# Kernel optimization log

Hardware: AMD Instinct MI355X
Metric: run time of the kernel (lower is better)

The kernel has to match this reference:

```python
import jax, jax.numpy as jnp
import numpy as np

EPS = 1e-9
ROUTINGS = 3
B, H, CIN, COUT = 16, 8, 32, 32


def setup_inputs() -> dict:
    key = jax.random.key(0)
    k1, k2 = jax.random.split(key)
    # activations/poses from a previous capsule layer are in [0,1) after squashing/sigmoid
    x = jax.random.uniform(k1, (B, H, H, CIN * 17), dtype=jnp.float32)
    w = jax.random.normal(k2, (1, CIN, COUT, 4, 4), dtype=jnp.float32)  # TruncatedNormal(std=1) ~ normal
    beta_v = jnp.zeros((COUT, 18), jnp.float32)
    beta_a = jnp.zeros((COUT,), jnp.float32)
    ij = jnp.stack(jnp.meshgrid(jnp.arange(H), jnp.arange(H), indexing='ij'), axis=-1)
    coord_add = ij.reshape(H * H, 2).astype(jnp.float32) / H  # [H*H, 2] scaled coords
    return {"x": x, "w": w, "beta_v": beta_v, "beta_a": beta_a, "coord_add": coord_add}


def em_routing(votes, activation, beta_v, beta_a, routings):
    # votes: [N, ci, co, ch=18], activation: [N, ci, 1]
    N, ci, co, ch = votes.shape
    r = jnp.full((N, ci, co), 1.0 / co, dtype=votes.dtype)
    miu = sigma_sq = act_out = None
    for it in range(routings):  # small fixed routing count
        if it > 0:
            # E-step: Gaussian log-likelihood of each vote under each output capsule
            log_p = -0.5 * jnp.log(sigma_sq) - jnp.square(votes - miu) / (2.0 * sigma_sq)  # [N,ci,co,ch]
            log_p = log_p - (jnp.max(log_p, axis=(2, 3), keepdims=True) - jnp.log(10.0))
            p = jnp.exp(jnp.sum(log_p, axis=3))  # [N,ci,co]
            ap = p * act_out.reshape(N, 1, co)
            r = ap / (jnp.sum(ap, axis=2, keepdims=True) + EPS)
        # M-step
        r = r * activation  # weight by input activation, broadcast over co
        r = r / (jnp.sum(r, axis=2, keepdims=True) + EPS)
        r_sum = jnp.sum(r, axis=1, keepdims=True)  # [N,1,co]
        r1 = (r / (r_sum + EPS))[..., None]        # [N,ci,co,1]
        miu = jnp.sum(votes * r1, axis=1, keepdims=True)                        # [N,1,co,ch]
        sigma_sq = jnp.sum(jnp.square(votes - miu) * r1, axis=1, keepdims=True) + EPS
        if it == routings - 1:
            rs = r_sum.reshape(N, co, 1)
            cost_h = (beta_v + 0.5 * jnp.log(sigma_sq.reshape(N, co, ch))) * rs  # [N,co,ch]
            ac_lambda = 0.01 * (it + 1)
            act_out = jax.nn.softmax(ac_lambda * (beta_a - jnp.sum(cost_h, axis=2)), axis=-1)
        else:
            act_out = jax.nn.softmax(r_sum.reshape(N, co), axis=-1)
    return miu, act_out


def reference(x, w, beta_v, beta_a, coord_add):
    Bx, Hx, Wx, C = x.shape
    ci = C // 17
    xr = x.reshape(Bx, Hx, Wx, ci, 17)
    pose = xr[..., :16].reshape(-1, ci, 16)   # [N, ci, 16], N = B*H*W
    act = xr[..., 16].reshape(-1, ci, 1)      # [N, ci, 1]
    N = pose.shape[0]
    co = w.shape[2]
    # mat_transform: batched 4x4 matmul pose @ w per (input capsule, output capsule)
    votes = jnp.einsum('niab,icbd->nicad', pose.reshape(N, ci, 4, 4), w[0]).reshape(N, ci, co, 16)
    # coordinate addition: 2 extra channels with spatial coords, tiled over batch/capsules
    coord = jnp.broadcast_to(coord_add.reshape(Hx * Wx, 1, 1, 2), (Hx * Wx, ci, co, 2))
    coord = jnp.tile(coord, (Bx, 1, 1, 1))    # [N, ci, co, 2]
    votes = jnp.concatenate([coord, votes], axis=3)  # [N, ci, co, 18]
    miu, act_out = em_routing(votes, act, beta_v, beta_a, ROUTINGS)
    # global average pool over the spatial grid
    outputs = jnp.mean(act_out.reshape(Bx, Hx, Wx, co), axis=(1, 2))                       # [B, co]
    pose_out = jnp.mean(miu.reshape(Bx, Hx, Wx, co * 18), axis=(1, 2)).reshape(Bx, co, 18)  # [B, co, 18]
    return outputs, pose_out
```

## Files before the change

### kernel.cpp

```cpp
#include <hip/hip_runtime.h>
#include <math.h>


#define CI 32
#define CO 32
#define CH 18
#define NPOS 1024
#define SP 19
#define OUT_ACT (16 * CO)

constexpr float EPSF = 1e-9f;
constexpr float LN10 = 2.302585092994046f;

__global__ __launch_bounds__(256) void zero_out_kernel(float* __restrict__ out, int n) {
    int i = blockIdx.x * 256 + threadIdx.x;
    if (i < n) out[i] = 0.0f;
}

__device__ __forceinline__ float bf_max32(float x) {
    #pragma unroll
    for (int m = 16; m >= 1; m >>= 1) x = fmaxf(x, __shfl_xor(x, m));
    return x;
}
__device__ __forceinline__ float bf_sum32(float x) {
    #pragma unroll
    for (int m = 16; m >= 1; m >>= 1) x += __shfl_xor(x, m);
    return x;
}

__global__ __launch_bounds__(256) void caps_em_kernel(
    const float* __restrict__ x,
    const float* __restrict__ w,
    const float* __restrict__ beta_v,
    const float* __restrict__ beta_a,
    const float* __restrict__ coord_add,
    float* __restrict__ out)
{
    const int n  = blockIdx.x;
    const int t  = threadIdx.x;
    const int c  = t & 31;
    const int ig = t >> 5;

    __shared__ float pose[CI][16];
    __shared__ float act_in[CI];
    __shared__ float P[8][CO];
    __shared__ float partial[8][CO * SP];
    __shared__ float miu_s[CO * SP];
    __shared__ float lsig_s[CO * SP];
    __shared__ float inv2_s[CO * SP];

    const float* xrow = x + n * (CI * 17);
    for (int e = t; e < CI * 17; e += 256) {
        int i = e / 17, k = e % 17;
        float val = xrow[e];
        if (k < 16) pose[i][k] = val;
        else        act_in[i]  = val;
    }
    const float cx = coord_add[(n & 63) * 2 + 0];
    const float cy = coord_add[(n & 63) * 2 + 1];
    __syncthreads();

    float v[4][16];
    float a_in[4];
    #pragma unroll
    for (int k = 0; k < 4; ++k) {
        int i = ig * 4 + k;
        a_in[k] = act_in[i];
        float pr[16], wr[16];
        const float4* pp4 = (const float4*)pose[i];
        const float4* wp4 = (const float4*)(w + ((i * CO + c) << 4));
        #pragma unroll
        for (int q = 0; q < 4; ++q) {
            float4 pf = pp4[q];
            pr[q*4+0] = pf.x; pr[q*4+1] = pf.y; pr[q*4+2] = pf.z; pr[q*4+3] = pf.w;
            float4 wf = wp4[q];
            wr[q*4+0] = wf.x; wr[q*4+1] = wf.y; wr[q*4+2] = wf.z; wr[q*4+3] = wf.w;
        }
        #pragma unroll
        for (int a = 0; a < 4; ++a) {
            #pragma unroll
            for (int d = 0; d < 4; ++d) {
                float s = pr[a*4+0] * wr[0*4+d];
                s += pr[a*4+1] * wr[1*4+d];
                s += pr[a*4+2] * wr[2*4+d];
                s += pr[a*4+3] * wr[3*4+d];
                v[k][a*4+d] = s;
            }
        }
    }

    float rr[4];
    float act_c = 0.0f;

    for (int it = 0; it < 3; ++it) {
        if (it > 0) {
            #pragma unroll
            for (int k = 0; k < 4; ++k) {
                float S = 0.0f, mx = -3.0e38f;
                #pragma unroll
                for (int ch = 0; ch < CH; ++ch) {
                    float vv = (ch == 0) ? cx : ((ch == 1) ? cy : v[k][ch - 2]);
                    float d  = vv - miu_s[c * SP + ch];
                    float lp = -0.5f * lsig_s[c * SP + ch] - d * d * inv2_s[c * SP + ch];
                    S += lp;
                    mx = fmaxf(mx, lp);
                }
                float m = bf_max32(mx);
                float shift = 18.0f * (m - LN10);
                float p  = expf(S - shift);
                float ap = p * act_c;
                float A  = bf_sum32(ap);
                float re = ap / (A + EPSF);
                float sk = A / (A + EPSF);
                float an = a_in[k];
                rr[k] = re * an / (an * sk + EPSF);
            }
        } else {
            #pragma unroll
            for (int k = 0; k < 4; ++k) {
                float an = a_in[k];
                rr[k] = (1.0f / 32.0f) * an / (an + EPSF);
            }
        }

        P[ig][c] = rr[0] + rr[1] + rr[2] + rr[3];
        __syncthreads();
        float r_sum = 0.0f;
        #pragma unroll
        for (int g = 0; g < 8; ++g) r_sum += P[g][c];
        float denom = r_sum + EPSF;
        float r1[4], r1s = 0.0f;
        #pragma unroll
        for (int k = 0; k < 4; ++k) { r1[k] = rr[k] / denom; r1s += r1[k]; }

        {
            float* pp = &partial[ig][c * SP];
            pp[0] = cx * r1s;
            pp[1] = cy * r1s;
            #pragma unroll
            for (int ch = 2; ch < CH; ++ch)
                pp[ch] = v[0][ch-2]*r1[0] + v[1][ch-2]*r1[1]
                       + v[2][ch-2]*r1[2] + v[3][ch-2]*r1[3];
        }
        __syncthreads();
        for (int e = t; e < CO * SP; e += 256) {
            float s = 0.0f;
            #pragma unroll
            for (int g = 0; g < 8; ++g) s += partial[g][e];
            miu_s[e] = s;
        }
        __syncthreads();

        {
            float* pp = &partial[ig][c * SP];
            float d0 = cx - miu_s[c * SP + 0];
            float d1 = cy - miu_s[c * SP + 1];
            pp[0] = d0 * d0 * r1s;
            pp[1] = d1 * d1 * r1s;
            #pragma unroll
            for (int ch = 2; ch < CH; ++ch) {
                float mu = miu_s[c * SP + ch];
                float e0 = v[0][ch-2]-mu, e1 = v[1][ch-2]-mu;
                float e2 = v[2][ch-2]-mu, e3 = v[3][ch-2]-mu;
                pp[ch] = e0*e0*r1[0] + e1*e1*r1[1] + e2*e2*r1[2] + e3*e3*r1[3];
            }
        }
        __syncthreads();
        for (int e = t; e < CO * SP; e += 256) {
            float s = 0.0f;
            #pragma unroll
            for (int g = 0; g < 8; ++g) s += partial[g][e];
            s += EPSF;
            lsig_s[e] = logf(s);
            inv2_s[e] = 0.5f / s;
        }
        __syncthreads();

        float logit;
        if (it == 2) {
            float cost = 0.0f;
            #pragma unroll
            for (int ch = 0; ch < CH; ++ch)
                cost += beta_v[c * CH + ch] + 0.5f * lsig_s[c * SP + ch];
            logit = 0.03f * (beta_a[c] - cost * r_sum);
        } else {
            logit = r_sum;
        }
        float mx = bf_max32(logit);
        float ex = expf(logit - mx);
        float sden = bf_sum32(ex);
        act_c = ex / sden;
    }

    const float inv64 = 1.0f / 64.0f;
    const int b = n >> 6;
    if (t < CO) atomicAdd(&out[b * CO + t], act_c * inv64);
    for (int e = t; e < CO * CH; e += 256) {
        int cc = e / CH, ch = e - cc * CH;
        atomicAdd(&out[OUT_ACT + b * (CO * CH) + e], miu_s[cc * SP + ch] * inv64);
    }
}

extern "C" void kernel_launch(void* const* d_in, const int* in_sizes, int n_in,
                              void* d_out, int out_size, void* d_ws, size_t ws_size,
                              hipStream_t stream) {
    const float* x         = (const float*)d_in[0];
    const float* w         = (const float*)d_in[1];
    const float* beta_v    = (const float*)d_in[2];
    const float* beta_a    = (const float*)d_in[3];
    const float* coord_add = (const float*)d_in[4];
    float* out = (float*)d_out;

    zero_out_kernel<<<dim3((out_size + 255) / 256), dim3(256), 0, stream>>>(out, out_size);
    caps_em_kernel<<<dim3(NPOS), dim3(256), 0, stream>>>(
        x, w, beta_v, beta_a, coord_add, out);
}
```

Measured before the change: 93.27 us.

## Fuse mean and variance into one pass via raw moments, cut barriers

The M-step now accumulates unnormalised first and second moments in a single pass. Variance is computed as E[v^2]-mu^2 with a correction factor, which removes one reduce round and two barriers per iteration. Partial sums are pre-combined across half-waves with shuffles, so shared memory holds 4 slices instead of 8. The E-step loop is reordered to load each channel's shared values once for all four capsules, fast __expf/__logf intrinsics are used, and the zeroing kernel is replaced by hipMemsetAsync. The one-pass variance can lose precision through cancellation, which the clamp to zero only partly masks.

```diff
diff --git a/kernel.cpp b/kernel.cpp
--- a/kernel.cpp
+++ b/kernel.cpp
@@ -6,16 +6,12 @@
 #define CO 32
 #define CH 18
 #define NPOS 1024
-#define SP 19
+#define PSTR 38
+#define MSTR 19
 #define OUT_ACT (16 * CO)
 
 constexpr float EPSF = 1e-9f;
 constexpr float LN10 = 2.302585092994046f;
-
-__global__ __launch_bounds__(256) void zero_out_kernel(float* __restrict__ out, int n) {
-    int i = blockIdx.x * 256 + threadIdx.x;
-    if (i < n) out[i] = 0.0f;
-}
 
 __device__ __forceinline__ float bf_max32(float x) {
     #pragma unroll
@@ -40,14 +36,14 @@
     const int t  = threadIdx.x;
     const int c  = t & 31;
     const int ig = t >> 5;
+    const int wv = t >> 6;
 
     __shared__ float pose[CI][16];
     __shared__ float act_in[CI];
-    __shared__ float P[8][CO];
-    __shared__ float partial[8][CO * SP];
-    __shared__ float miu_s[CO * SP];
-    __shared__ float lsig_s[CO * SP];
-    __shared__ float inv2_s[CO * SP];
+    __shared__ float part[4][CO * PSTR];
+    __shared__ float miu_s[CO * MSTR];
+    __shared__ float lsig_s[CO * MSTR];
+    __shared__ float inv2_s[CO * MSTR];
 
     const float* xrow = x + n * (CI * 17);
     for (int e = t; e < CI * 17; e += 256) {
@@ -94,24 +90,32 @@
 
     for (int it = 0; it < 3; ++it) {
         if (it > 0) {
+            float S[4]  = {0.0f, 0.0f, 0.0f, 0.0f};
+            float mx[4] = {-3.0e38f, -3.0e38f, -3.0e38f, -3.0e38f};
+            #pragma unroll
+            for (int ch = 0; ch < CH; ++ch) {
+                float mu   = miu_s[c * MSTR + ch];
+                float base = -0.5f * lsig_s[c * MSTR + ch];
+                float q    = inv2_s[c * MSTR + ch];
+                #pragma unroll
+                for (int k = 0; k < 4; ++k) {
+                    float vv = (ch == 0) ? cx : ((ch == 1) ? cy : v[k][ch - 2]);
+                    float d  = vv - mu;
+                    float lp = base - d * d * q;
+                    S[k] += lp;
+                    mx[k] = fmaxf(mx[k], lp);
+                }
+            }
             #pragma unroll
             for (int k = 0; k < 4; ++k) {
-                float S = 0.0f, mx = -3.0e38f;
-                #pragma unroll
-                for (int ch = 0; ch < CH; ++ch) {
-                    float vv = (ch == 0) ? cx : ((ch == 1) ? cy : v[k][ch - 2]);
-                    float d  = vv - miu_s[c * SP + ch];
-                    float lp = -0.5f * lsig_s[c * SP + ch] - d * d * inv2_s[c * SP + ch];
-                    S += lp;
-                    mx = fmaxf(mx, lp);
-                }
-                float m = bf_max32(mx);
+                float m = bf_max32(mx[k]);
                 float shift = 18.0f * (m - LN10);
-                float p  = expf(S - shift);
+                float p  = __expf(S[k] - shift);
                 float ap = p * act_c;
                 float A  = bf_sum32(ap);
-                float re = ap / (A + EPSF);
-                float sk = A / (A + EPSF);
+                float invA = 1.0f / (A + EPSF);
+                float re = ap * invA;
+                float sk = A * invA;
                 float an = a_in[k];
                 rr[k] = re * an / (an * sk + EPSF);
             }
@@ -123,56 +127,51 @@
             }
         }
 
-        P[ig][c] = rr[0] + rr[1] + rr[2] + rr[3];
+        {
+            float* pp = &part[wv][c * PSTR];
+            float prr = rr[0] + rr[1] + rr[2] + rr[3];
+            float prs = prr + __shfl_xor(prr, 32);
+            pp[0] = prs;
+            float s0 = cx * prr, s1v = cy * prr;
+            s0  += __shfl_xor(s0, 32);
+            s1v += __shfl_xor(s1v, 32);
+            pp[1] = s0;  pp[19] = cx * s0;
+            pp[2] = s1v; pp[20] = cy * s1v;
+            #pragma unroll
+            for (int ch = 2; ch < CH; ++ch) {
+                float s = 0.0f, s2 = 0.0f;
+                #pragma unroll
+                for (int k = 0; k < 4; ++k) {
+                    float rv = rr[k] * v[k][ch - 2];
+                    s  += rv;
+                    s2 += rv * v[k][ch - 2];
+                }
+                s  += __shfl_xor(s, 32);
+                s2 += __shfl_xor(s2, 32);
+                pp[1 + ch]  = s;
+                pp[19 + ch] = s2;
+            }
+        }
         __syncthreads();
-        float r_sum = 0.0f;
-        #pragma unroll
-        for (int g = 0; g < 8; ++g) r_sum += P[g][c];
-        float denom = r_sum + EPSF;
-        float r1[4], r1s = 0.0f;
-        #pragma unroll
-        for (int k = 0; k < 4; ++k) { r1[k] = rr[k] / denom; r1s += r1[k]; }
-
+
+        float r_sum;
         {
-            float* pp = &partial[ig][c * SP];
-            pp[0] = cx * r1s;
-            pp[1] = cy * r1s;
-            #pragma unroll
-            for (int ch = 2; ch < CH; ++ch)
-                pp[ch] = v[0][ch-2]*r1[0] + v[1][ch-2]*r1[1]
-                       + v[2][ch-2]*r1[2] + v[3][ch-2]*r1[3];
-        }
-        __syncthreads();
-        for (int e = t; e < CO * SP; e += 256) {
-            float s = 0.0f;
-            #pragma unroll
-            for (int g = 0; g < 8; ++g) s += partial[g][e];
-            miu_s[e] = s;
-        }
-        __syncthreads();
-
-        {
-            float* pp = &partial[ig][c * SP];
-            float d0 = cx - miu_s[c * SP + 0];
-            float d1 = cy - miu_s[c * SP + 1];
-            pp[0] = d0 * d0 * r1s;
-            pp[1] = d1 * d1 * r1s;
-            #pragma unroll
-            for (int ch = 2; ch < CH; ++ch) {
-                float mu = miu_s[c * SP + ch];
-                float e0 = v[0][ch-2]-mu, e1 = v[1][ch-2]-mu;
-                float e2 = v[2][ch-2]-mu, e3 = v[3][ch-2]-mu;
-                pp[ch] = e0*e0*r1[0] + e1*e1*r1[1] + e2*e2*r1[2] + e3*e3*r1[3];
-            }
-        }
-        __syncthreads();
-        for (int e = t; e < CO * SP; e += 256) {
-            float s = 0.0f;
-            #pragma unroll
-            for (int g = 0; g < 8; ++g) s += partial[g][e];
-            s += EPSF;
-            lsig_s[e] = logf(s);
-            inv2_s[e] = 0.5f / s;
+            const int base = c * PSTR;
+            float rs = part[0][base] + part[1][base] + part[2][base] + part[3][base];
+            r_sum = rs;
+            float rsinv = 1.0f / (rs + EPSF);
+            float s1 = rs * rsinv;
+            float c2 = 2.0f - s1;
+            for (int ch = ig; ch < CH; ch += 8) {
+                int jm = base + 1 + ch, jv = base + 19 + ch;
+                float mu_un = part[0][jm] + part[1][jm] + part[2][jm] + part[3][jm];
+                float v2_un = part[0][jv] + part[1][jv] + part[2][jv] + part[3][jv];
+                float mu = mu_un * rsinv;
+                float sig = fmaxf(v2_un * rsinv - mu * mu * c2, 0.0f) + EPSF;
+                miu_s[c * MSTR + ch]  = mu;
+                lsig_s[c * MSTR + ch] = __logf(sig);
+                inv2_s[c * MSTR + ch] = 0.5f / sig;
+            }
         }
         __syncthreads();
 
@@ -181,15 +180,14 @@
             float cost = 0.0f;
             #pragma unroll
             for (int ch = 0; ch < CH; ++ch)
-                cost += beta_v[c * CH + ch] + 0.5f * lsig_s[c * SP + ch];
+                cost += beta_v[c * CH + ch] + 0.5f * lsig_s[c * MSTR + ch];
             logit = 0.03f * (beta_a[c] - cost * r_sum);
         } else {
             logit = r_sum;
         }
-        float mx = bf_max32(logit);
-        float ex = expf(logit - mx);
-        float sden = bf_sum32(ex);
-        act_c = ex / sden;
+        float mxl = bf_max32(logit);
+        float ex  = __expf(logit - mxl);
+        act_c = ex / bf_sum32(ex);
     }
 
     const float inv64 = 1.0f / 64.0f;
@@ -197,7 +195,7 @@
     if (t < CO) atomicAdd(&out[b * CO + t], act_c * inv64);
     for (int e = t; e < CO * CH; e += 256) {
         int cc = e / CH, ch = e - cc * CH;
-        atomicAdd(&out[OUT_ACT + b * (CO * CH) + e], miu_s[cc * SP + ch] * inv64);
+        atomicAdd(&out[OUT_ACT + b * (CO * CH) + e], miu_s[cc * MSTR + ch] * inv64);
     }
 }
 
@@ -211,7 +209,7 @@
     const float* coord_add = (const float*)d_in[4];
     float* out = (float*)d_out;
 
-    zero_out_kernel<<<dim3((out_size + 255) / 256), dim3(256), 0, stream>>>(out, out_size);
+    hipMemsetAsync(out, 0, (size_t)out_size * sizeof(float), stream);
     caps_em_kernel<<<dim3(NPOS), dim3(256), 0, stream>>>(
         x, w, beta_v, beta_a, coord_add, out);
 }
```

Result: no change. 94.49 us (+1.3%).
